# Optimization experiments

Measured on AMD Instinct MI355X. Metric: run time of the kernel, lower is better.

## Reference

```python
import jax, jax.numpy as jnp
import numpy as np

N_NODES = 100000
N_EDGES = 1600000
EMB = 128
EDGE_DIMS = [6, 3]
BN_EPS = 1e-5


def setup_inputs() -> dict:
    key = jax.random.key(0)
    ks = jax.random.split(key, 16)
    inp = {
        "node_feats": jax.random.normal(ks[0], (N_NODES, EMB), jnp.float32),
        "edge_feat_0": jax.random.uniform(ks[1], (N_EDGES, EDGE_DIMS[0]), jnp.float32),
        "edge_feat_1": jax.random.uniform(ks[2], (N_EDGES, EDGE_DIMS[1]), jnp.float32),
        "src": jax.random.randint(ks[3], (N_EDGES,), 0, N_NODES, jnp.int32),
        "dst": jax.random.randint(ks[4], (N_EDGES,), 0, N_NODES, jnp.int32),
    }
    # edge embedding linears (MLP num_layers==1 -> plain Linear)
    s0 = 1.0 / np.sqrt(EDGE_DIMS[0])
    s1 = 1.0 / np.sqrt(EDGE_DIMS[1])
    inp["We0"] = jax.random.uniform(ks[5], (EDGE_DIMS[0], EMB), jnp.float32, -s0, s0)
    inp["be0"] = jax.random.uniform(ks[6], (EMB,), jnp.float32, -s0, s0)
    inp["We1"] = jax.random.uniform(ks[7], (EDGE_DIMS[1], EMB), jnp.float32, -s1, s1)
    inp["be1"] = jax.random.uniform(ks[8], (EMB,), jnp.float32, -s1, s1)
    # mlp: Linear(emb, 2*emb) -> ReLU -> Linear(2*emb, emb)
    sm = 1.0 / np.sqrt(EMB)
    sh = 1.0 / np.sqrt(2 * EMB)
    inp["W1"] = jax.random.uniform(ks[9], (EMB, 2 * EMB), jnp.float32, -sm, sm)
    inp["b1"] = jax.random.uniform(ks[10], (2 * EMB,), jnp.float32, -sm, sm)
    inp["W2"] = jax.random.uniform(ks[11], (2 * EMB, EMB), jnp.float32, -sh, sh)
    inp["b2"] = jax.random.uniform(ks[12], (EMB,), jnp.float32, -sh, sh)
    # batch norm affine params
    inp["gamma"] = jnp.ones((EMB,), jnp.float32)
    inp["beta"] = jnp.zeros((EMB,), jnp.float32)
    return inp


def reference(node_feats, edge_feat_0, edge_feat_1, src, dst,
              We0, be0, We1, be1, W1, b1, W2, b2, gamma, beta):
    n_nodes = node_feats.shape[0]
    # per-family edge embeddings, summed
    edge_embs = (edge_feat_0 @ We0 + be0) + (edge_feat_1 @ We1 + be1)  # [E, D]
    # u_add_e: gather src node feats, add edge emb
    msgs = node_feats[src] + edge_embs  # [E, D]
    # scatter-sum to destination nodes
    agg = jax.ops.segment_sum(msgs, dst, num_segments=n_nodes)  # [N, D]
    # MLP: Linear -> ReLU -> Linear
    h = jax.nn.relu(agg @ W1 + b1) @ W2 + b2  # [N, D]
    # BatchNorm1d (training mode: batch statistics, biased variance)
    mean = jnp.mean(h, axis=0)
    var = jnp.var(h, axis=0)
    h = (h - mean) * jax.lax.rsqrt(var + BN_EPS) * gamma + beta
    return h
```

## Files before the change

### kernel.cpp

```cpp
#include <hip/hip_runtime.h>

#define N_NODES 100000
#define N_EDGES 1600000
#define EMB 128
#define BM 16
#define NSLAB 64
#define BN_EPS 1e-5f

#define SCAN_BLK 512
#define NB_SCAN ((N_NODES + SCAN_BLK - 1) / SCAN_BLK)
#define NPAD (NB_SCAN * SCAN_BLK)
#define RECW 10

typedef short short8 __attribute__((ext_vector_type(8)));
typedef float floatx4 __attribute__((ext_vector_type(4)));

__device__ __forceinline__ ushort f2bf(float x) {
    unsigned u = __float_as_uint(x);
    u += 0x7fffu + ((u >> 16) & 1u);
    return (ushort)(u >> 16);
}


__global__ __launch_bounds__(256) void hist_kernel(
    const int* __restrict__ dst, int* __restrict__ counts)
{
    int e = blockIdx.x * 256 + threadIdx.x;
    if (e < N_EDGES) atomicAdd(&counts[dst[e]], 1);
}

__global__ __launch_bounds__(SCAN_BLK) void scan_blocksum_kernel(
    const int* __restrict__ counts, int* __restrict__ blockSums)
{
    __shared__ int red[SCAN_BLK];
    int t = threadIdx.x;
    int i = blockIdx.x * SCAN_BLK + t;
    red[t] = (i < N_NODES) ? counts[i] : 0;
    __syncthreads();
    for (int s = SCAN_BLK / 2; s > 0; s >>= 1) {
        if (t < s) red[t] += red[t + s];
        __syncthreads();
    }
    if (t == 0) blockSums[blockIdx.x] = red[0];
}

__global__ __launch_bounds__(256) void scan_blockoffsets_kernel(int* __restrict__ blockSums)
{
    __shared__ int s[256];
    int t = threadIdx.x;
    int orig = (t < NB_SCAN) ? blockSums[t] : 0;
    s[t] = orig;
    __syncthreads();
    for (int off = 1; off < 256; off <<= 1) {
        int v = (t >= off) ? s[t - off] : 0;
        __syncthreads();
        s[t] += v;
        __syncthreads();
    }
    if (t < NB_SCAN) blockSums[t] = s[t] - orig;
}

__global__ __launch_bounds__(SCAN_BLK) void scan_final_kernel(
    const int* __restrict__ counts, const int* __restrict__ blockSums,
    int* __restrict__ offsets, int* __restrict__ cursor)
{
    __shared__ int s[SCAN_BLK];
    int t = threadIdx.x;
    int i = blockIdx.x * SCAN_BLK + t;
    int orig = (i < N_NODES) ? counts[i] : 0;
    s[t] = orig;
    __syncthreads();
    for (int off = 1; off < SCAN_BLK; off <<= 1) {
        int v = (t >= off) ? s[t - off] : 0;
        __syncthreads();
        s[t] += v;
        __syncthreads();
    }
    int excl = s[t] - orig + blockSums[blockIdx.x];
    if (i < N_NODES) { offsets[i] = excl; cursor[i] = excl; }
    if (i == N_NODES) offsets[N_NODES] = N_EDGES;
}

__global__ __launch_bounds__(256) void scatter_rec_kernel(
    const int* __restrict__ src, const int* __restrict__ dst,
    const float* __restrict__ ef0, const float* __restrict__ ef1,
    int* __restrict__ cursor, float* __restrict__ recF)
{
    int e = blockIdx.x * 256 + threadIdx.x;
    if (e >= N_EDGES) return;
    int pos = atomicAdd(&cursor[dst[e]], 1);
    float r[RECW];
    r[0] = __int_as_float(src[e]);
    const float2* f0 = (const float2*)(ef0 + (long)e * 6);
    float2 a = f0[0], b = f0[1], c = f0[2];
    r[1] = a.x; r[2] = a.y; r[3] = b.x; r[4] = b.y; r[5] = c.x; r[6] = c.y;
    r[7] = ef1[(long)e * 3 + 0];
    r[8] = ef1[(long)e * 3 + 1];
    r[9] = ef1[(long)e * 3 + 2];
    float* out = recF + (long)pos * RECW;
#pragma unroll
    for (int j = 0; j < RECW; ++j) out[j] = r[j];
}

__global__ __launch_bounds__(256) void gather_rec_kernel(
    const float* __restrict__ node_feats,
    const float* __restrict__ recF, const int* __restrict__ offsets,
    const float* __restrict__ We0, const float* __restrict__ be0,
    const float* __restrict__ We1, const float* __restrict__ be1,
    float* __restrict__ agg)
{
    int wave = threadIdx.x >> 6;
    int lane = threadIdx.x & 63;
    int n = blockIdx.x * 4 + wave;
    if (n >= N_NODES) return;

    float2 w[9];
#pragma unroll
    for (int k = 0; k < 6; ++k) w[k] = ((const float2*)We0)[k * 64 + lane];
#pragma unroll
    for (int k = 0; k < 3; ++k) w[6 + k] = ((const float2*)We1)[k * 64 + lane];
    float2 bias;
    {
        float2 a = ((const float2*)be0)[lane];
        float2 b = ((const float2*)be1)[lane];
        bias.x = a.x + b.x; bias.y = a.y + b.y;
    }

    int beg = offsets[n];
    int end = offsets[n + 1];
    int col = lane % 10;
    float colsum = 0.f;
    float2 acc = make_float2(0.f, 0.f);
    const float2* nf2 = (const float2*)node_feats;

    for (int base = beg; base < end; base += 6) {
        int m = end - base; if (m > 6) m = 6;
        float v = 0.f;
        if (lane < m * 10) v = recF[(long)base * RECW + lane];
        if (col != 0) colsum += v;
#pragma unroll 6
        for (int j = 0; j < 6; ++j) {
            if (j >= m) break;
            int s = __float_as_int(__shfl(v, j * 10));
            float2 nf = nf2[(long)s * 64 + lane];
            acc.x += nf.x;
            acc.y += nf.y;
        }
    }

    float s1 = colsum + __shfl(colsum, lane + 30);
    float tot = s1 + __shfl(s1, lane + 10) + __shfl(s1, lane + 20);

    float deg = (float)(end - beg);
    float2 emb = make_float2(deg * bias.x, deg * bias.y);
#pragma unroll
    for (int k = 0; k < 9; ++k) {
        float fk = __shfl(tot, k + 1);
        emb.x = fmaf(fk, w[k].x, emb.x);
        emb.y = fmaf(fk, w[k].y, emb.y);
    }
    acc.x += emb.x;
    acc.y += emb.y;
    ((float2*)agg)[(long)n * 64 + lane] = acc;
}

__global__ __launch_bounds__(256) void scatter_kernel(
    const int* __restrict__ src, const int* __restrict__ dst,
    int* __restrict__ cursor, int2* __restrict__ sorted)
{
    int e = blockIdx.x * 256 + threadIdx.x;
    if (e >= N_EDGES) return;
    int t = dst[e];
    int pos = atomicAdd(&cursor[t], 1);
    sorted[pos] = make_int2(src[e], e);
}

__global__ __launch_bounds__(256) void gather_reduce_kernel(
    const float* __restrict__ node_feats,
    const float* __restrict__ ef0, const float* __restrict__ ef1,
    const int2* __restrict__ sorted, const int* __restrict__ offsets,
    const float* __restrict__ We0, const float* __restrict__ be0,
    const float* __restrict__ We1, const float* __restrict__ be1,
    float* __restrict__ agg)
{
    int wave = threadIdx.x >> 6;
    int lane = threadIdx.x & 63;
    int n = blockIdx.x * 4 + wave;
    if (n >= N_NODES) return;

    float2 w0[6], w1[3];
#pragma unroll
    for (int k = 0; k < 6; ++k) w0[k] = ((const float2*)We0)[k * 64 + lane];
#pragma unroll
    for (int k = 0; k < 3; ++k) w1[k] = ((const float2*)We1)[k * 64 + lane];
    float2 bias;
    {
        float2 a = ((const float2*)be0)[lane];
        float2 b = ((const float2*)be1)[lane];
        bias.x = a.x + b.x; bias.y = a.y + b.y;
    }

    int beg = offsets[n];
    int end = offsets[n + 1];
    float2 acc = make_float2(0.f, 0.f);

    for (int i = beg; i < end; ++i) {
        int2 se = sorted[i];
        float f = 0.f;
        if (lane < 6)      f = ef0[(long)se.y * 6 + lane];
        else if (lane < 9) f = ef1[(long)se.y * 3 + (lane - 6)];

        float2 emb = bias;
#pragma unroll
        for (int k = 0; k < 6; ++k) {
            float fk = __shfl(f, k);
            emb.x = fmaf(fk, w0[k].x, emb.x);
            emb.y = fmaf(fk, w0[k].y, emb.y);
        }
#pragma unroll
        for (int k = 0; k < 3; ++k) {
            float fk = __shfl(f, 6 + k);
            emb.x = fmaf(fk, w1[k].x, emb.x);
            emb.y = fmaf(fk, w1[k].y, emb.y);
        }
        float2 nf = ((const float2*)node_feats)[(long)se.x * 64 + lane];
        acc.x += nf.x + emb.x;
        acc.y += nf.y + emb.y;
    }
    ((float2*)agg)[(long)n * 64 + lane] = acc;
}

__global__ __launch_bounds__(256) void edge_scatter_kernel(
    const float* __restrict__ node_feats,
    const float* __restrict__ ef0,
    const float* __restrict__ ef1,
    const int* __restrict__ src,
    const int* __restrict__ dst,
    const float* __restrict__ We0, const float* __restrict__ be0,
    const float* __restrict__ We1, const float* __restrict__ be1,
    float* __restrict__ agg)
{
    __shared__ float wS[10 * EMB];
    int tid = threadIdx.x;
    for (int i = tid; i < 6 * EMB; i += 256) wS[i] = We0[i];
    for (int i = tid; i < 3 * EMB; i += 256) wS[6 * EMB + i] = We1[i];
    if (tid < EMB) wS[9 * EMB + tid] = be0[tid] + be1[tid];
    __syncthreads();

    int e = blockIdx.x * 2 + (tid >> 7);
    if (e >= N_EDGES) return;
    int d = tid & 127;
    int s = src[e];
    int t = dst[e];
    const float* f0 = ef0 + (long)e * 6;
    const float* f1 = ef1 + (long)e * 3;

    float emb = wS[9 * EMB + d];
#pragma unroll
    for (int k = 0; k < 6; ++k) emb = fmaf(f0[k], wS[k * EMB + d], emb);
#pragma unroll
    for (int k = 0; k < 3; ++k) emb = fmaf(f1[k], wS[6 * EMB + k * EMB + d], emb);

    float val = node_feats[(long)s * EMB + d] + emb;
    atomicAdd(&agg[(long)t * EMB + d], val);
}

__global__ __launch_bounds__(256) void prep_frags_kernel(
    const float* __restrict__ W1, const float* __restrict__ W2,
    ushort* __restrict__ w1f, ushort* __restrict__ w2f)
{
    int idx = blockIdx.x * 256 + threadIdx.x;
    int i = idx & 7;
    int lane = (idx >> 3) & 63;
    int kloc = ((lane >> 4) << 3) + i;
    int nloc = lane & 15;
    if (idx < 32768) {
        int ks = (idx >> 9) & 3, nt = idx >> 11;
        w1f[idx] = f2bf(W1[(ks * 32 + kloc) * 256 + nt * 16 + nloc]);
    } else {
        int j = idx - 32768;
        int ks = (j >> 9) & 7, nt = j >> 12;
        w2f[j] = f2bf(W2[(ks * 32 + kloc) * 128 + nt * 16 + nloc]);
    }
}

__global__ __launch_bounds__(256) void mlp_mfma_kernel(
    float* __restrict__ h,
    const ushort* __restrict__ w1f, const ushort* __restrict__ w2f,
    const float* __restrict__ b1, const float* __restrict__ b2,
    float* __restrict__ stats)
{
    __shared__ __align__(16) char aggS[32 * 256];
    __shared__ __align__(16) char h1S[32 * 512];

    int tid = threadIdx.x;
    int lane = tid & 63;
    int wv = tid >> 6;
    long base = (long)blockIdx.x * 32;

    for (int c = tid; c < 32 * 16; c += 256) {
        int row = c >> 4, j = c & 15;
        const float4* g = (const float4*)(h + (base + row) * EMB + j * 8);
        float4 x = g[0], y = g[1];
        union { ushort u[8]; short8 v; } pk;
        pk.u[0] = f2bf(x.x); pk.u[1] = f2bf(x.y); pk.u[2] = f2bf(x.z); pk.u[3] = f2bf(x.w);
        pk.u[4] = f2bf(y.x); pk.u[5] = f2bf(y.y); pk.u[6] = f2bf(y.z); pk.u[7] = f2bf(y.w);
        *(short8*)&aggS[row * 256 + ((j * 16) ^ ((row & 7) << 4))] = pk.v;
    }
    __syncthreads();

    floatx4 acc1[2][4];
#pragma unroll
    for (int nt = 0; nt < 4; ++nt) {
        float bias = b1[(wv * 4 + nt) * 16 + (lane & 15)];
#pragma unroll
        for (int mt = 0; mt < 2; ++mt)
            acc1[mt][nt] = (floatx4){bias, bias, bias, bias};
    }
    int swz = (lane & 7) << 4;
#pragma unroll
    for (int ks = 0; ks < 4; ++ks) {
        int kb = ks * 64 + ((lane >> 4) << 4);
        short8 a0 = *(const short8*)&aggS[(lane & 15) * 256 + (kb ^ swz)];
        short8 a1 = *(const short8*)&aggS[(16 + (lane & 15)) * 256 + (kb ^ swz)];
#pragma unroll
        for (int nt = 0; nt < 4; ++nt) {
            short8 b = *(const short8*)&w1f[(((wv * 4 + nt) * 4 + ks) * 64 + lane) * 8];
            acc1[0][nt] = __builtin_amdgcn_mfma_f32_16x16x32_bf16(a0, b, acc1[0][nt], 0, 0, 0);
            acc1[1][nt] = __builtin_amdgcn_mfma_f32_16x16x32_bf16(a1, b, acc1[1][nt], 0, 0, 0);
        }
    }
#pragma unroll
    for (int mt = 0; mt < 2; ++mt)
#pragma unroll
        for (int nt = 0; nt < 4; ++nt)
#pragma unroll
            for (int i = 0; i < 4; ++i) {
                int row = mt * 16 + ((lane >> 4) << 2) + i;
                int col = (wv * 4 + nt) * 16 + (lane & 15);
                float v = fmaxf(acc1[mt][nt][i], 0.f);
                *(ushort*)&h1S[row * 512 + ((2 * col) ^ ((row & 7) << 4))] = f2bf(v);
            }
    __syncthreads();

    floatx4 acc2[2][2];
#pragma unroll
    for (int nt = 0; nt < 2; ++nt) {
        float bias = b2[(wv * 2 + nt) * 16 + (lane & 15)];
#pragma unroll
        for (int mt = 0; mt < 2; ++mt)
            acc2[mt][nt] = (floatx4){bias, bias, bias, bias};
    }
#pragma unroll
    for (int ks = 0; ks < 8; ++ks) {
        int kb = ks * 64 + ((lane >> 4) << 4);
        short8 a0 = *(const short8*)&h1S[(lane & 15) * 512 + (kb ^ swz)];
        short8 a1 = *(const short8*)&h1S[(16 + (lane & 15)) * 512 + (kb ^ swz)];
#pragma unroll
        for (int nt = 0; nt < 2; ++nt) {
            short8 b = *(const short8*)&w2f[(((wv * 2 + nt) * 8 + ks) * 64 + lane) * 8];
            acc2[0][nt] = __builtin_amdgcn_mfma_f32_16x16x32_bf16(a0, b, acc2[0][nt], 0, 0, 0);
            acc2[1][nt] = __builtin_amdgcn_mfma_f32_16x16x32_bf16(a1, b, acc2[1][nt], 0, 0, 0);
        }
    }

    float s[2] = {0.f, 0.f}, s2[2] = {0.f, 0.f};
#pragma unroll
    for (int nt = 0; nt < 2; ++nt) {
        int col = (wv * 2 + nt) * 16 + (lane & 15);
#pragma unroll
        for (int mt = 0; mt < 2; ++mt)
#pragma unroll
            for (int i = 0; i < 4; ++i) {
                int row = mt * 16 + ((lane >> 4) << 2) + i;
                float v = acc2[mt][nt][i];
                h[(base + row) * EMB + col] = v;
                s[nt] += v;
                s2[nt] = fmaf(v, v, s2[nt]);
            }
    }
#pragma unroll
    for (int nt = 0; nt < 2; ++nt) {
        s[nt] += __shfl_xor(s[nt], 16);
        s[nt] += __shfl_xor(s[nt], 32);
        s2[nt] += __shfl_xor(s2[nt], 16);
        s2[nt] += __shfl_xor(s2[nt], 32);
    }
    if (lane < 16) {
        float* slab = stats + (blockIdx.x & (NSLAB - 1)) * (2 * EMB);
#pragma unroll
        for (int nt = 0; nt < 2; ++nt) {
            int col = (wv * 2 + nt) * 16 + lane;
            atomicAdd(&slab[col], s[nt]);
            atomicAdd(&slab[EMB + col], s2[nt]);
        }
    }
}

__global__ __launch_bounds__(256) void mlp_kernel(
    float* __restrict__ h,
    const float* __restrict__ W1, const float* __restrict__ b1,
    const float* __restrict__ W2, const float* __restrict__ b2,
    float* __restrict__ stats)
{
    __shared__ float aggS[BM][EMB];
    __shared__ float h1S[BM][2 * EMB];
    __shared__ float sredS[256];
    __shared__ float s2redS[256];

    int tid = threadIdx.x;
    long base = (long)blockIdx.x * BM;

    for (int i = tid; i < BM * EMB; i += 256)
        aggS[i >> 7][i & 127] = h[base * EMB + i];
    __syncthreads();

    {
        float acc[BM];
        float bias = b1[tid];
#pragma unroll
        for (int r = 0; r < BM; ++r) acc[r] = bias;
        for (int k = 0; k < EMB; ++k) {
            float w = W1[k * (2 * EMB) + tid];
#pragma unroll
            for (int r = 0; r < BM; ++r) acc[r] = fmaf(aggS[r][k], w, acc[r]);
        }
#pragma unroll
        for (int r = 0; r < BM; ++r) h1S[r][tid] = fmaxf(acc[r], 0.0f);
    }
    __syncthreads();

    {
        int c = tid & 127;
        int half = tid >> 7;
        float acc[8];
        float bias = b2[c];
#pragma unroll
        for (int r = 0; r < 8; ++r) acc[r] = bias;
        for (int k = 0; k < 2 * EMB; ++k) {
            float w = W2[k * EMB + c];
#pragma unroll
            for (int r = 0; r < 8; ++r) acc[r] = fmaf(h1S[half * 8 + r][k], w, acc[r]);
        }
        float s = 0.f, s2 = 0.f;
#pragma unroll
        for (int r = 0; r < 8; ++r) {
            h[(base + half * 8 + r) * EMB + c] = acc[r];
            s += acc[r];
            s2 = fmaf(acc[r], acc[r], s2);
        }
        sredS[tid] = s;
        s2redS[tid] = s2;
    }
    __syncthreads();
    if (tid < 128) {
        float s = sredS[tid] + sredS[tid + 128];
        float s2 = s2redS[tid] + s2redS[tid + 128];
        float* slab = stats + (blockIdx.x & (NSLAB - 1)) * (2 * EMB);
        atomicAdd(&slab[tid], s);
        atomicAdd(&slab[EMB + tid], s2);
    }
}

__global__ __launch_bounds__(128) void bn_finalize_kernel(
    const float* __restrict__ stats,
    const float* __restrict__ gamma, const float* __restrict__ beta,
    float* __restrict__ scaleshift)
{
    int c = threadIdx.x;
    float s = 0.f, s2 = 0.f;
    for (int b = 0; b < NSLAB; ++b) {
        s += stats[b * (2 * EMB) + c];
        s2 += stats[b * (2 * EMB) + EMB + c];
    }
    float mean = s / (float)N_NODES;
    float var = s2 / (float)N_NODES - mean * mean;
    float sc = gamma[c] * rsqrtf(var + BN_EPS);
    scaleshift[c] = sc;
    scaleshift[EMB + c] = beta[c] - mean * sc;
}

__global__ __launch_bounds__(256) void bn_apply_kernel(
    float* __restrict__ h, const float* __restrict__ scaleshift)
{
    __shared__ float scS[EMB], shS[EMB];
    if (threadIdx.x < EMB) {
        scS[threadIdx.x] = scaleshift[threadIdx.x];
        shS[threadIdx.x] = scaleshift[EMB + threadIdx.x];
    }
    __syncthreads();
    long total = (long)N_NODES * EMB / 4;
    long stride = (long)gridDim.x * blockDim.x;
    for (long i = (long)blockIdx.x * blockDim.x + threadIdx.x; i < total; i += stride) {
        float4 v = ((float4*)h)[i];
        int c = (int)((i * 4) & 127);
        v.x = fmaf(v.x, scS[c + 0], shS[c + 0]);
        v.y = fmaf(v.y, scS[c + 1], shS[c + 1]);
        v.z = fmaf(v.z, scS[c + 2], shS[c + 2]);
        v.w = fmaf(v.w, scS[c + 3], shS[c + 3]);
        ((float4*)h)[i] = v;
    }
}

extern "C" void kernel_launch(void* const* d_in, const int* in_sizes, int n_in,
                              void* d_out, int out_size, void* d_ws, size_t ws_size,
                              hipStream_t stream) {
    const float* node_feats = (const float*)d_in[0];
    const float* ef0 = (const float*)d_in[1];
    const float* ef1 = (const float*)d_in[2];
    const int* src = (const int*)d_in[3];
    const int* dst = (const int*)d_in[4];
    const float* We0 = (const float*)d_in[5];
    const float* be0 = (const float*)d_in[6];
    const float* We1 = (const float*)d_in[7];
    const float* be1 = (const float*)d_in[8];
    const float* W1 = (const float*)d_in[9];
    const float* b1 = (const float*)d_in[10];
    const float* W2 = (const float*)d_in[11];
    const float* b2 = (const float*)d_in[12];
    const float* gamma = (const float*)d_in[13];
    const float* beta = (const float*)d_in[14];

    float* out = (float*)d_out;

    float* stats = (float*)d_ws;
    float* scaleshift = stats + NSLAB * 2 * EMB;
    int* counts = (int*)(scaleshift + 256);
    int* offsets = counts + NPAD;
    int* cursor = offsets + NPAD;
    int* blockSums = cursor + NPAD;
    float* recF = (float*)(blockSums + 256);
    int2* sorted = (int2*)(blockSums + 256);
    ushort* w1f_rec = (ushort*)recF;
    ushort* w2f_rec = w1f_rec + 32768;
    ushort* w1f_mid = (ushort*)(sorted + N_EDGES);
    ushort* w2f_mid = w1f_mid + 32768;

    size_t needRec = (size_t)((char*)(recF + (size_t)N_EDGES * RECW) - (char*)d_ws);
    size_t needSorted = (size_t)((char*)(w2f_mid + 32768) - (char*)d_ws);

    hipMemsetAsync(stats, 0, (size_t)NSLAB * 2 * EMB * sizeof(float), stream);

    if (ws_size >= needSorted) {
        hipMemsetAsync(counts, 0, (size_t)N_NODES * sizeof(int), stream);
        hist_kernel<<<(N_EDGES + 255) / 256, 256, 0, stream>>>(dst, counts);
        scan_blocksum_kernel<<<NB_SCAN, SCAN_BLK, 0, stream>>>(counts, blockSums);
        scan_blockoffsets_kernel<<<1, 256, 0, stream>>>(blockSums);
        scan_final_kernel<<<NB_SCAN, SCAN_BLK, 0, stream>>>(counts, blockSums, offsets, cursor);
        ushort* w1f; ushort* w2f;
        if (ws_size >= needRec) {
            scatter_rec_kernel<<<(N_EDGES + 255) / 256, 256, 0, stream>>>(
                src, dst, ef0, ef1, cursor, recF);
            gather_rec_kernel<<<(N_NODES + 3) / 4, 256, 0, stream>>>(
                node_feats, recF, offsets, We0, be0, We1, be1, out);
            w1f = w1f_rec; w2f = w2f_rec;
        } else {
            scatter_kernel<<<(N_EDGES + 255) / 256, 256, 0, stream>>>(src, dst, cursor, sorted);
            gather_reduce_kernel<<<(N_NODES + 3) / 4, 256, 0, stream>>>(
                node_feats, ef0, ef1, sorted, offsets, We0, be0, We1, be1, out);
            w1f = w1f_mid; w2f = w2f_mid;
        }
        prep_frags_kernel<<<256, 256, 0, stream>>>(W1, W2, w1f, w2f);
        mlp_mfma_kernel<<<N_NODES / 32, 256, 0, stream>>>(out, w1f, w2f, b1, b2, stats);
    } else {
        hipMemsetAsync(d_out, 0, (size_t)N_NODES * EMB * sizeof(float), stream);
        edge_scatter_kernel<<<N_EDGES / 2, 256, 0, stream>>>(
            node_feats, ef0, ef1, src, dst, We0, be0, We1, be1, out);
        mlp_kernel<<<N_NODES / BM, 256, 0, stream>>>(out, W1, b1, W2, b2, stats);
    }

    bn_finalize_kernel<<<1, 128, 0, stream>>>(stats, gamma, beta, scaleshift);
    bn_apply_kernel<<<2048, 256, 0, stream>>>(out, scaleshift);
}
```

Measured before the change: 375.8 us.

## Gather bf16 node features, atomically presum edge features, feed bf16 agg to MLP

Node features are converted to bf16 once, so the per-edge neighbour gather reads half the bytes, with two edges handled per wave iteration. The sorted record buffer is replaced by a src-only index array plus per-node atomic sums of the 9 edge features, shrinking the scatter writes. The aggregate is written directly as bf16 and the MLP loads it straight into MFMA fragments, skipping the fp32 round trip and LDS staging. The costs are 9 float atomics per edge, extra conversion and memset passes, and lower precision in the gathered sum.

Result: slower. 1.047 ms (+178.7%).

```diff
diff --git a/kernel.cpp b/kernel.cpp
--- a/kernel.cpp
+++ b/kernel.cpp
@@ -10,7 +10,6 @@
 #define SCAN_BLK 512
 #define NB_SCAN ((N_NODES + SCAN_BLK - 1) / SCAN_BLK)
 #define NPAD (NB_SCAN * SCAN_BLK)
-#define RECW 10
 
 typedef short short8 __attribute__((ext_vector_type(8)));
 typedef float floatx4 __attribute__((ext_vector_type(4)));
@@ -19,6 +18,9 @@
     unsigned u = __float_as_uint(x);
     u += 0x7fffu + ((u >> 16) & 1u);
     return (ushort)(u >> 16);
+}
+__device__ __forceinline__ float bf2f(ushort u) {
+    return __uint_as_float(((unsigned)u) << 16);
 }
 
 
@@ -81,153 +83,106 @@
     if (i == N_NODES) offsets[N_NODES] = N_EDGES;
 }
 
-__global__ __launch_bounds__(256) void scatter_rec_kernel(
+__global__ __launch_bounds__(256) void cvt_nf_kernel(
+    const float* __restrict__ nf, ushort* __restrict__ nfbf)
+{
+    long total = (long)N_NODES * EMB / 4;
+    long stride = (long)gridDim.x * 256;
+    for (long p = blockIdx.x * 256L + threadIdx.x; p < total; p += stride) {
+        float4 v = ((const float4*)nf)[p];
+        ushort4 o;
+        o.x = f2bf(v.x); o.y = f2bf(v.y); o.z = f2bf(v.z); o.w = f2bf(v.w);
+        ((ushort4*)nfbf)[p] = o;
+    }
+}
+
+__global__ __launch_bounds__(256) void scatter_fs_kernel(
     const int* __restrict__ src, const int* __restrict__ dst,
     const float* __restrict__ ef0, const float* __restrict__ ef1,
-    int* __restrict__ cursor, float* __restrict__ recF)
-{
-    int e = blockIdx.x * 256 + threadIdx.x;
-    if (e >= N_EDGES) return;
-    int pos = atomicAdd(&cursor[dst[e]], 1);
-    float r[RECW];
-    r[0] = __int_as_float(src[e]);
-    const float2* f0 = (const float2*)(ef0 + (long)e * 6);
-    float2 a = f0[0], b = f0[1], c = f0[2];
-    r[1] = a.x; r[2] = a.y; r[3] = b.x; r[4] = b.y; r[5] = c.x; r[6] = c.y;
-    r[7] = ef1[(long)e * 3 + 0];
-    r[8] = ef1[(long)e * 3 + 1];
-    r[9] = ef1[(long)e * 3 + 2];
-    float* out = recF + (long)pos * RECW;
-#pragma unroll
-    for (int j = 0; j < RECW; ++j) out[j] = r[j];
-}
-
-__global__ __launch_bounds__(256) void gather_rec_kernel(
-    const float* __restrict__ node_feats,
-    const float* __restrict__ recF, const int* __restrict__ offsets,
-    const float* __restrict__ We0, const float* __restrict__ be0,
-    const float* __restrict__ We1, const float* __restrict__ be1,
-    float* __restrict__ agg)
-{
-    int wave = threadIdx.x >> 6;
-    int lane = threadIdx.x & 63;
-    int n = blockIdx.x * 4 + wave;
-    if (n >= N_NODES) return;
-
-    float2 w[9];
-#pragma unroll
-    for (int k = 0; k < 6; ++k) w[k] = ((const float2*)We0)[k * 64 + lane];
-#pragma unroll
-    for (int k = 0; k < 3; ++k) w[6 + k] = ((const float2*)We1)[k * 64 + lane];
-    float2 bias;
-    {
-        float2 a = ((const float2*)be0)[lane];
-        float2 b = ((const float2*)be1)[lane];
-        bias.x = a.x + b.x; bias.y = a.y + b.y;
-    }
-
-    int beg = offsets[n];
-    int end = offsets[n + 1];
-    int col = lane % 10;
-    float colsum = 0.f;
-    float2 acc = make_float2(0.f, 0.f);
-    const float2* nf2 = (const float2*)node_feats;
-
-    for (int base = beg; base < end; base += 6) {
-        int m = end - base; if (m > 6) m = 6;
-        float v = 0.f;
-        if (lane < m * 10) v = recF[(long)base * RECW + lane];
-        if (col != 0) colsum += v;
-#pragma unroll 6
-        for (int j = 0; j < 6; ++j) {
-            if (j >= m) break;
-            int s = __float_as_int(__shfl(v, j * 10));
-            float2 nf = nf2[(long)s * 64 + lane];
-            acc.x += nf.x;
-            acc.y += nf.y;
-        }
-    }
-
-    float s1 = colsum + __shfl(colsum, lane + 30);
-    float tot = s1 + __shfl(s1, lane + 10) + __shfl(s1, lane + 20);
-
-    float deg = (float)(end - beg);
-    float2 emb = make_float2(deg * bias.x, deg * bias.y);
-#pragma unroll
-    for (int k = 0; k < 9; ++k) {
-        float fk = __shfl(tot, k + 1);
-        emb.x = fmaf(fk, w[k].x, emb.x);
-        emb.y = fmaf(fk, w[k].y, emb.y);
-    }
-    acc.x += emb.x;
-    acc.y += emb.y;
-    ((float2*)agg)[(long)n * 64 + lane] = acc;
-}
-
-__global__ __launch_bounds__(256) void scatter_kernel(
-    const int* __restrict__ src, const int* __restrict__ dst,
-    int* __restrict__ cursor, int2* __restrict__ sorted)
+    int* __restrict__ cursor, int* __restrict__ srcS, float* __restrict__ fsum)
 {
     int e = blockIdx.x * 256 + threadIdx.x;
     if (e >= N_EDGES) return;
     int t = dst[e];
     int pos = atomicAdd(&cursor[t], 1);
-    sorted[pos] = make_int2(src[e], e);
-}
-
-__global__ __launch_bounds__(256) void gather_reduce_kernel(
-    const float* __restrict__ node_feats,
-    const float* __restrict__ ef0, const float* __restrict__ ef1,
-    const int2* __restrict__ sorted, const int* __restrict__ offsets,
+    srcS[pos] = src[e];
+    float* fs = fsum + (long)t * 16;
+    const float2* f0 = (const float2*)(ef0 + (long)e * 6);
+    float2 a = f0[0], b = f0[1], c = f0[2];
+    atomicAdd(&fs[0], a.x); atomicAdd(&fs[1], a.y);
+    atomicAdd(&fs[2], b.x); atomicAdd(&fs[3], b.y);
+    atomicAdd(&fs[4], c.x); atomicAdd(&fs[5], c.y);
+    atomicAdd(&fs[6], ef1[(long)e * 3 + 0]);
+    atomicAdd(&fs[7], ef1[(long)e * 3 + 1]);
+    atomicAdd(&fs[8], ef1[(long)e * 3 + 2]);
+}
+
+__global__ __launch_bounds__(256) void gather_bf_kernel(
+    const ushort* __restrict__ nfbf, const int* __restrict__ srcS,
+    const int* __restrict__ offsets, const float* __restrict__ fsum,
     const float* __restrict__ We0, const float* __restrict__ be0,
     const float* __restrict__ We1, const float* __restrict__ be1,
-    float* __restrict__ agg)
-{
-    int wave = threadIdx.x >> 6;
-    int lane = threadIdx.x & 63;
-    int n = blockIdx.x * 4 + wave;
+    ushort* __restrict__ aggbf)
+{
+    int wv = threadIdx.x >> 6, lane = threadIdx.x & 63;
+    int n = blockIdx.x * 4 + wv;
     if (n >= N_NODES) return;
-
-    float2 w0[6], w1[3];
-#pragma unroll
-    for (int k = 0; k < 6; ++k) w0[k] = ((const float2*)We0)[k * 64 + lane];
-#pragma unroll
-    for (int k = 0; k < 3; ++k) w1[k] = ((const float2*)We1)[k * 64 + lane];
-    float2 bias;
-    {
-        float2 a = ((const float2*)be0)[lane];
-        float2 b = ((const float2*)be1)[lane];
-        bias.x = a.x + b.x; bias.y = a.y + b.y;
-    }
-
-    int beg = offsets[n];
-    int end = offsets[n + 1];
-    float2 acc = make_float2(0.f, 0.f);
-
-    for (int i = beg; i < end; ++i) {
-        int2 se = sorted[i];
-        float f = 0.f;
-        if (lane < 6)      f = ef0[(long)se.y * 6 + lane];
-        else if (lane < 9) f = ef1[(long)se.y * 3 + (lane - 6)];
-
-        float2 emb = bias;
-#pragma unroll
-        for (int k = 0; k < 6; ++k) {
-            float fk = __shfl(f, k);
-            emb.x = fmaf(fk, w0[k].x, emb.x);
-            emb.y = fmaf(fk, w0[k].y, emb.y);
-        }
-#pragma unroll
-        for (int k = 0; k < 3; ++k) {
-            float fk = __shfl(f, 6 + k);
-            emb.x = fmaf(fk, w1[k].x, emb.x);
-            emb.y = fmaf(fk, w1[k].y, emb.y);
-        }
-        float2 nf = ((const float2*)node_feats)[(long)se.x * 64 + lane];
-        acc.x += nf.x + emb.x;
-        acc.y += nf.y + emb.y;
-    }
-    ((float2*)agg)[(long)n * 64 + lane] = acc;
+    int half = lane >> 5, lp = lane & 31;
+
+    float4 w[9];
+#pragma unroll
+    for (int k = 0; k < 6; ++k) w[k] = ((const float4*)We0)[k * 32 + lp];
+#pragma unroll
+    for (int k = 0; k < 3; ++k) w[6 + k] = ((const float4*)We1)[k * 32 + lp];
+    float4 ba = ((const float4*)be0)[lp];
+    float4 bb = ((const float4*)be1)[lp];
+
+    int beg = offsets[n], end = offsets[n + 1];
+    float4 acc = make_float4(0.f, 0.f, 0.f, 0.f);
+    const ushort4* nf4 = (const ushort4*)nfbf;
+
+    for (int base = beg; base < end; base += 64) {
+        int m = end - base; if (m > 64) m = 64;
+        int sid = 0;
+        if (lane < m) sid = srcS[base + lane];
+        int it = (m + 1) >> 1;
+        for (int j = 0; j < it; ++j) {
+            int r = 2 * j + half;
+            int s = __shfl(sid, r);
+            if (r < m) {
+                ushort4 nv = nf4[(long)s * 32 + lp];
+                acc.x += bf2f(nv.x); acc.y += bf2f(nv.y);
+                acc.z += bf2f(nv.z); acc.w += bf2f(nv.w);
+            }
+        }
+    }
+    acc.x += __shfl_xor(acc.x, 32);
+    acc.y += __shfl_xor(acc.y, 32);
+    acc.z += __shfl_xor(acc.z, 32);
+    acc.w += __shfl_xor(acc.w, 32);
+
+    float f = (lane < 9) ? fsum[(long)n * 16 + lane] : 0.f;
+    float fk[9];
+#pragma unroll
+    for (int k = 0; k < 9; ++k) fk[k] = __shfl(f, k);
+
+    if (half == 0) {
+        float deg = (float)(end - beg);
+        float4 emb;
+        emb.x = deg * (ba.x + bb.x); emb.y = deg * (ba.y + bb.y);
+        emb.z = deg * (ba.z + bb.z); emb.w = deg * (ba.w + bb.w);
+#pragma unroll
+        for (int k = 0; k < 9; ++k) {
+            emb.x = fmaf(fk[k], w[k].x, emb.x);
+            emb.y = fmaf(fk[k], w[k].y, emb.y);
+            emb.z = fmaf(fk[k], w[k].z, emb.z);
+            emb.w = fmaf(fk[k], w[k].w, emb.w);
+        }
+        ushort4 o;
+        o.x = f2bf(acc.x + emb.x); o.y = f2bf(acc.y + emb.y);
+        o.z = f2bf(acc.z + emb.z); o.w = f2bf(acc.w + emb.w);
+        ((ushort4*)aggbf)[(long)n * 32 + lp] = o;
+    }
 }
 
 __global__ __launch_bounds__(256) void edge_scatter_kernel(
@@ -285,12 +240,11 @@
 }
 
 __global__ __launch_bounds__(256) void mlp_mfma_kernel(
-    float* __restrict__ h,
+    const ushort* __restrict__ aggbf, float* __restrict__ h,
     const ushort* __restrict__ w1f, const ushort* __restrict__ w2f,
     const float* __restrict__ b1, const float* __restrict__ b2,
     float* __restrict__ stats)
 {
-    __shared__ __align__(16) char aggS[32 * 256];
     __shared__ __align__(16) char h1S[32 * 512];
 
     int tid = threadIdx.x;
@@ -298,16 +252,14 @@
     int wv = tid >> 6;
     long base = (long)blockIdx.x * 32;
 
-    for (int c = tid; c < 32 * 16; c += 256) {
-        int row = c >> 4, j = c & 15;
-        const float4* g = (const float4*)(h + (base + row) * EMB + j * 8);
-        float4 x = g[0], y = g[1];
-        union { ushort u[8]; short8 v; } pk;
-        pk.u[0] = f2bf(x.x); pk.u[1] = f2bf(x.y); pk.u[2] = f2bf(x.z); pk.u[3] = f2bf(x.w);
-        pk.u[4] = f2bf(y.x); pk.u[5] = f2bf(y.y); pk.u[6] = f2bf(y.z); pk.u[7] = f2bf(y.w);
-        *(short8*)&aggS[row * 256 + ((j * 16) ^ ((row & 7) << 4))] = pk.v;
-    }
-    __syncthreads();
+    short8 a[2][4];
+#pragma unroll
+    for (int mt = 0; mt < 2; ++mt)
+#pragma unroll
+        for (int ks = 0; ks < 4; ++ks) {
+            long row = base + mt * 16 + (lane & 15);
+            a[mt][ks] = *(const short8*)&aggbf[row * EMB + ks * 32 + ((lane >> 4) << 3)];
+        }
 
     floatx4 acc1[2][4];
 #pragma unroll
@@ -317,17 +269,13 @@
         for (int mt = 0; mt < 2; ++mt)
             acc1[mt][nt] = (floatx4){bias, bias, bias, bias};
     }
-    int swz = (lane & 7) << 4;
 #pragma unroll
     for (int ks = 0; ks < 4; ++ks) {
-        int kb = ks * 64 + ((lane >> 4) << 4);
-        short8 a0 = *(const short8*)&aggS[(lane & 15) * 256 + (kb ^ swz)];
-        short8 a1 = *(const short8*)&aggS[(16 + (lane & 15)) * 256 + (kb ^ swz)];
 #pragma unroll
         for (int nt = 0; nt < 4; ++nt) {
             short8 b = *(const short8*)&w1f[(((wv * 4 + nt) * 4 + ks) * 64 + lane) * 8];
-            acc1[0][nt] = __builtin_amdgcn_mfma_f32_16x16x32_bf16(a0, b, acc1[0][nt], 0, 0, 0);
-            acc1[1][nt] = __builtin_amdgcn_mfma_f32_16x16x32_bf16(a1, b, acc1[1][nt], 0, 0, 0);
+            acc1[0][nt] = __builtin_amdgcn_mfma_f32_16x16x32_bf16(a[0][ks], b, acc1[0][nt], 0, 0, 0);
+            acc1[1][nt] = __builtin_amdgcn_mfma_f32_16x16x32_bf16(a[1][ks], b, acc1[1][nt], 0, 0, 0);
         }
     }
 #pragma unroll
@@ -343,6 +291,7 @@
             }
     __syncthreads();
 
+    int swz = (lane & 7) << 4;
     floatx4 acc2[2][2];
 #pragma unroll
     for (int nt = 0; nt < 2; ++nt) {
@@ -529,39 +478,31 @@
     int* offsets = counts + NPAD;
     int* cursor = offsets + NPAD;
     int* blockSums = cursor + NPAD;
-    float* recF = (float*)(blockSums + 256);
-    int2* sorted = (int2*)(blockSums + 256);
-    ushort* w1f_rec = (ushort*)recF;
-    ushort* w2f_rec = w1f_rec + 32768;
-    ushort* w1f_mid = (ushort*)(sorted + N_EDGES);
-    ushort* w2f_mid = w1f_mid + 32768;
-
-    size_t needRec = (size_t)((char*)(recF + (size_t)N_EDGES * RECW) - (char*)d_ws);
-    size_t needSorted = (size_t)((char*)(w2f_mid + 32768) - (char*)d_ws);
+    ushort* w1f = (ushort*)(blockSums + 256);
+    ushort* w2f = w1f + 32768;
+    float* fsum = (float*)(w2f + 32768);
+    int* srcS = (int*)(fsum + (size_t)N_NODES * 16);
+    ushort* nfbf = (ushort*)(srcS + N_EDGES);
+    ushort* aggbf = nfbf + (size_t)N_NODES * EMB;
+    size_t needed = (size_t)((char*)(aggbf + (size_t)N_NODES * EMB) - (char*)d_ws);
 
     hipMemsetAsync(stats, 0, (size_t)NSLAB * 2 * EMB * sizeof(float), stream);
 
-    if (ws_size >= needSorted) {
+    if (ws_size >= needed) {
         hipMemsetAsync(counts, 0, (size_t)N_NODES * sizeof(int), stream);
+        hipMemsetAsync(fsum, 0, (size_t)N_NODES * 16 * sizeof(float), stream);
+        cvt_nf_kernel<<<2048, 256, 0, stream>>>(node_feats, nfbf);
         hist_kernel<<<(N_EDGES + 255) / 256, 256, 0, stream>>>(dst, counts);
         scan_blocksum_kernel<<<NB_SCAN, SCAN_BLK, 0, stream>>>(counts, blockSums);
         scan_blockoffsets_kernel<<<1, 256, 0, stream>>>(blockSums);
         scan_final_kernel<<<NB_SCAN, SCAN_BLK, 0, stream>>>(counts, blockSums, offsets, cursor);
-        ushort* w1f; ushort* w2f;
-        if (ws_size >= needRec) {
-            scatter_rec_kernel<<<(N_EDGES + 255) / 256, 256, 0, stream>>>(
-                src, dst, ef0, ef1, cursor, recF);
-            gather_rec_kernel<<<(N_NODES + 3) / 4, 256, 0, stream>>>(
-                node_feats, recF, offsets, We0, be0, We1, be1, out);
-            w1f = w1f_rec; w2f = w2f_rec;
-        } else {
-            scatter_kernel<<<(N_EDGES + 255) / 256, 256, 0, stream>>>(src, dst, cursor, sorted);
-            gather_reduce_kernel<<<(N_NODES + 3) / 4, 256, 0, stream>>>(
-                node_feats, ef0, ef1, sorted, offsets, We0, be0, We1, be1, out);
-            w1f = w1f_mid; w2f = w2f_mid;
-        }
+        scatter_fs_kernel<<<(N_EDGES + 255) / 256, 256, 0, stream>>>(
+            src, dst, ef0, ef1, cursor, srcS, fsum);
+        gather_bf_kernel<<<(N_NODES + 3) / 4, 256, 0, stream>>>(
+            nfbf, srcS, offsets, fsum, We0, be0, We1, be1, aggbf);
         prep_frags_kernel<<<256, 256, 0, stream>>>(W1, W2, w1f, w2f);
-        mlp_mfma_kernel<<<N_NODES / 32, 256, 0, stream>>>(out, w1f, w2f, b1, b2, stats);
+        mlp_mfma_kernel<<<N_NODES / 32, 256, 0, stream>>>(
+            aggbf, out, w1f, w2f, b1, b2, stats);
     } else {
         hipMemsetAsync(d_out, 0, (size_t)N_NODES * EMB * sizeof(float), stream);
         edge_scatter_kernel<<<N_EDGES / 2, 256, 0, stream>>>(
@@ -570,5 +511,5 @@
     }
 
     bn_finalize_kernel<<<1, 128, 0, stream>>>(stats, gamma, beta, scaleshift);
-    bn_apply_kernel<<<2048, 256, 0, stream>>>(out, scaleshift);
-}
+    bn_apply_kernel<<<4096, 256, 0, stream>>>(out, scaleshift);
+}
```
